# Performance work log

Measured on AMD Instinct MI355X. Metric: run time of the kernel, lower is better.

## Reference

```python
import jax, jax.numpy as jnp
import numpy as np
import math

def _eq_conv1x1(x, w):
    # EqualizedConv2d: 1x1 conv, no bias, weight scaled by sqrt(2 / fan_in) at runtime.
    scale = math.sqrt(2.0 / w.shape[1])
    return jnp.einsum('bchw,oc->bohw', x, w * scale)

def _maxpool2x2(x):
    b, c, h, w = x.shape
    return x.reshape(b, c, h // 2, 2, w // 2, 2).max(axis=(3, 5))

def setup_inputs() -> dict:
    key = jax.random.key(0)
    ks = jax.random.split(key, 6)
    B, Cin, H, W = 8, 256, 64, 64
    Cout = 512
    return {
        'x': jax.random.normal(ks[0], (B, Cin, H, W), dtype=jnp.float32),
        'w_theta': jax.random.normal(ks[1], (Cout // 8, Cin), dtype=jnp.float32),
        'w_phi': jax.random.normal(ks[2], (Cout // 8, Cin), dtype=jnp.float32),
        'w_g': jax.random.normal(ks[3], (Cout // 2, Cin), dtype=jnp.float32),
        'w_o': jax.random.normal(ks[4], (Cout, Cout // 2), dtype=jnp.float32),
        'w_res': jax.random.normal(ks[5], (Cout, Cin), dtype=jnp.float32),
        'gamma': jnp.ones((1,), dtype=jnp.float32),
    }

def reference(x, w_theta, w_phi, w_g, w_o, w_res, gamma):
    B, _, H, W = x.shape
    theta = _eq_conv1x1(x, w_theta).reshape(B, -1, H * W)          # [B, Co/8, HW]
    phi = _maxpool2x2(_eq_conv1x1(x, w_phi)).reshape(B, -1, H * W // 4)  # [B, Co/8, HW/4]
    g = _maxpool2x2(_eq_conv1x1(x, w_g)).reshape(B, -1, H * W // 4)      # [B, Co/2, HW/4]
    # attention: softmax over key dim (no 1/sqrt(d) scaling, as in the original)
    scores = jnp.einsum('bcn,bcm->bnm', theta, phi)                # [B, HW, HW/4]
    beta = jax.nn.softmax(scores, axis=-1)
    att = jnp.einsum('bcm,bnm->bcn', g, beta).reshape(B, -1, H, W)  # [B, Co/2, H, W]
    out = _eq_conv1x1(att, w_o)                                     # [B, Co, H, W]
    res = _eq_conv1x1(x, w_res)
    inv_sqrt2 = jnp.float32(1.0 / math.sqrt(2.0))
    return (gamma[0] * out + res) * inv_sqrt2
```

## Files before the change

kernel.cpp:

```cpp
#include <hip/hip_runtime.h>


typedef _Float16 f16;
typedef f16 f16x2 __attribute__((ext_vector_type(2)));
typedef f16 f16x4 __attribute__((ext_vector_type(4)));
typedef f16 f16x8 __attribute__((ext_vector_type(8)));
typedef float f32x4 __attribute__((ext_vector_type(4)));

#define MFMA16(a, b, c) __builtin_amdgcn_mfma_f32_16x16x32_f16((a), (b), (c), 0, 0, 0)

__device__ __forceinline__ void gload16(const void* src, void* dst_lds) {
  __builtin_amdgcn_global_load_lds(
      (const __attribute__((address_space(1))) void*)src,
      (__attribute__((address_space(3))) void*)dst_lds, 16, 0, 0);
}

__global__ __launch_bounds__(256, 4)
void k_prep_w(const float* __restrict__ wt, const float* __restrict__ wp,
              const float* __restrict__ wg, const float* __restrict__ wo,
              const float* __restrict__ wr, const float* __restrict__ gamma,
              f16* __restrict__ Wproj, f16* __restrict__ Wcat) {
  int i = blockIdx.x * 256 + threadIdx.x;
  const float s = 0.08838834764831845f;
  const float is2 = 0.7071067811865476f;
  if (i < 384 * 256) {
    float v = (i < 64 * 256) ? wt[i]
              : (i < 128 * 256 ? wp[i - 64 * 256] : wg[i - 128 * 256]);
    Wproj[i] = (f16)(v * s);
  } else {
    int j = i - 384 * 256;
    if (j < 512 * 512) {
      int r = j >> 9, c = j & 511;
      float v = (c < 256) ? wo[r * 256 + c] * (gamma[0] * s * is2)
                          : wr[r * 256 + (c - 256)] * (s * is2);
      Wcat[j] = (f16)v;
    }
  }
}

__global__ __launch_bounds__(256, 4)
void k_transpose(const float* __restrict__ x, f16* __restrict__ xT) {
  __shared__ f16 tile[64 * 72];
  int b = blockIdx.z, nt = blockIdx.y, ct = blockIdx.x;
  int t = threadIdx.x;
  {
    int c = t >> 2, nch = (t & 3) * 16;
    const float* src = x + (((size_t)b * 256 + ct * 64 + c) << 12) + nt * 64 + nch;
    float4 v0 = *(const float4*)(src);
    float4 v1 = *(const float4*)(src + 4);
    float4 v2 = *(const float4*)(src + 8);
    float4 v3 = *(const float4*)(src + 12);
    f16x8 a = {(f16)v0.x, (f16)v0.y, (f16)v0.z, (f16)v0.w,
               (f16)v1.x, (f16)v1.y, (f16)v1.z, (f16)v1.w};
    f16x8 bb = {(f16)v2.x, (f16)v2.y, (f16)v2.z, (f16)v2.w,
                (f16)v3.x, (f16)v3.y, (f16)v3.z, (f16)v3.w};
    *(f16x8*)&tile[c * 72 + nch] = a;
    *(f16x8*)&tile[c * 72 + nch + 8] = bb;
  }
  __syncthreads();
  {
    int n = t >> 2, cch = (t & 3) * 16;
    f16 tmp[16];
#pragma unroll
    for (int i = 0; i < 16; i++) tmp[i] = tile[(cch + i) * 72 + n];
    f16x8 a, bb;
#pragma unroll
    for (int i = 0; i < 8; i++) { a[i] = tmp[i]; bb[i] = tmp[8 + i]; }
    f16* dst = xT + (((size_t)b * 4096 + nt * 64 + n) << 8) + ct * 64 + cch;
    *(f16x8*)dst = a;
    *(f16x8*)(dst + 8) = bb;
  }
}

__global__ __launch_bounds__(256, 2)
void k_gemm_projq(const f16* __restrict__ xT, const f16* __restrict__ Wproj,
                  f16* __restrict__ Q, f16* __restrict__ Kp, f16* __restrict__ V) {
  __shared__ f16 lds[192 * 64];
  f16* Alds = lds;
  f16* Blds = lds + 64 * 64;
  int b = blockIdx.z, mt = blockIdx.y, nt = blockIdx.x;
  int tid = threadIdx.x;
  int lane = tid & 63, wave = tid >> 6;
  int wm = wave >> 1, wn = wave & 1;
  int l15 = lane & 15, hi = lane >> 4;
  f32x4 acc[2][4];
#pragma unroll
  for (int mf = 0; mf < 2; mf++)
#pragma unroll
    for (int nf = 0; nf < 4; nf++) acc[mf][nf] = (f32x4){0, 0, 0, 0};
  const f16* Abase = Wproj + ((mt * 64) << 8);
  const f16* Bbase = xT + (((size_t)b * 4096 + nt * 128) << 8);
  for (int k0 = 0; k0 < 256; k0 += 64) {
    __syncthreads();
#pragma unroll
    for (int i = 0; i < 2; i++) {
      int chunk = i * 256 + tid;
      int row = chunk >> 3, cc = chunk & 7, scc = cc ^ (row & 7);
      gload16(Abase + (row << 8) + k0 + scc * 8, (char*)Alds + (i * 256 + wave * 64) * 16);
    }
#pragma unroll
    for (int i = 0; i < 4; i++) {
      int chunk = i * 256 + tid;
      int row = chunk >> 3, cc = chunk & 7, scc = cc ^ (row & 7);
      gload16(Bbase + (row << 8) + k0 + scc * 8, (char*)Blds + (i * 256 + wave * 64) * 16);
    }
    __syncthreads();
#pragma unroll
    for (int ks = 0; ks < 2; ks++) {
      int cb = (hi * 8 + ks * 32) * 2;
      f16x8 af[2], bf[4];
#pragma unroll
      for (int mf = 0; mf < 2; mf++) {
        int row = wm * 32 + mf * 16 + l15;
        af[mf] = *(const f16x8*)((const char*)Alds + row * 128 + (cb ^ ((row & 7) << 4)));
      }
#pragma unroll
      for (int nf = 0; nf < 4; nf++) {
        int row = wn * 64 + nf * 16 + l15;
        bf[nf] = *(const f16x8*)((const char*)Blds + row * 128 + (cb ^ ((row & 7) << 4)));
      }
#pragma unroll
      for (int mf = 0; mf < 2; mf++)
#pragma unroll
        for (int nf = 0; nf < 4; nf++) acc[mf][nf] = MFMA16(af[mf], bf[nf], acc[mf][nf]);
    }
  }
  if (mt == 0) {
#pragma unroll
    for (int mf = 0; mf < 2; mf++)
#pragma unroll
      for (int nf = 0; nf < 4; nf++)
#pragma unroll
        for (int r = 0; r < 4; r++) {
          int jl = wm * 32 + mf * 16 + hi * 4 + r;
          int n = nt * 128 + wn * 64 + nf * 16 + l15;
          Q[(((size_t)b * 4096 + n) << 6) + jl] = (f16)acc[mf][nf][r];
        }
  } else {
    __syncthreads();
    f16* Pool = lds;
#pragma unroll
    for (int mf = 0; mf < 2; mf++)
#pragma unroll
      for (int nf = 0; nf < 4; nf++)
#pragma unroll
        for (int r = 0; r < 4; r++) {
          int jl = wm * 32 + mf * 16 + hi * 4 + r;
          int col = wn * 64 + nf * 16 + l15;
          Pool[jl * 132 + col] = (f16)acc[mf][nf][r];
        }
    __syncthreads();
    if (mt == 1) {
      int m_l = tid >> 3;
      int jj8 = (tid & 7) * 8;
      f16x8 w;
#pragma unroll
      for (int i = 0; i < 8; i++) {
        int jj = jj8 + i;
        f16x2 p0 = *(const f16x2*)&Pool[jj * 132 + 2 * m_l];
        f16x2 p1 = *(const f16x2*)&Pool[jj * 132 + 64 + 2 * m_l];
        float v = fmaxf(fmaxf((float)p0[0], (float)p0[1]),
                        fmaxf((float)p1[0], (float)p1[1]));
        w[i] = (f16)v;
      }
      *(f16x8*)&Kp[((size_t)b * 1024 + nt * 32 + m_l) * 64 + jj8] = w;
    } else {
      int ch_l = tid >> 2;
      int m8 = (tid & 3) * 8;
      f16x8 w;
#pragma unroll
      for (int i = 0; i < 8; i++) {
        int mm = m8 + i;
        f16x2 p0 = *(const f16x2*)&Pool[ch_l * 132 + 2 * mm];
        f16x2 p1 = *(const f16x2*)&Pool[ch_l * 132 + 64 + 2 * mm];
        float v = fmaxf(fmaxf((float)p0[0], (float)p0[1]),
                        fmaxf((float)p1[0], (float)p1[1]));
        w[i] = (f16)v;
      }
      int ch = (mt - 2) * 64 + ch_l;
      *(f16x8*)&V[(((size_t)b * 256 + ch) << 10) + nt * 32 + m8] = w;
    }
  }
}

__global__ __launch_bounds__(512, 4)
void k_flash(const f16* __restrict__ Q, const f16* __restrict__ Kp,
             const f16* __restrict__ V, f16* __restrict__ att) {
  __shared__ f16 Klds[64 * 64];
  __shared__ f16 Vlds[256 * 64];
  __shared__ f16 Plds[4][16 * 72];
  int b = blockIdx.y, qt = blockIdx.x;
  int tid = threadIdx.x;
  int lane = tid & 63, wave = tid >> 6;
  int rg = wave >> 1, cg2 = wave & 1;
  int l15 = lane & 15, hi = lane >> 4;
  const f16* Kb = Kp + ((size_t)b << 16);
  const f16* Vb = V + ((size_t)b << 18);
  f16* Pw = &Plds[rg][0];
  const float L2E = 1.44269504f;
  int krow_s = tid >> 3, kcc = tid & 7;
  int kscc = kcc ^ (krow_s & 7);
  const f16* kp_src = Kb + (krow_s << 6) + kscc * 8;
  f16* kp_dst = &Klds[tid * 8];
  const f16* vp_src[4];
  f16* vp_dst[4];
#pragma unroll
  for (int i = 0; i < 4; i++) {
    int chunk = i * 512 + tid;
    int row = chunk >> 3, cc = chunk & 7, scc = cc ^ (row & 7);
    vp_src[i] = Vb + ((size_t)row << 10) + scc * 8;
    vp_dst[i] = &Vlds[chunk * 8];
  }
  f16x8 qf[2];
#pragma unroll
  for (int ks = 0; ks < 2; ks++)
    qf[ks] = *(const f16x8*)(
        Q + (((size_t)b * 4096 + qt * 64 + rg * 16 + l15) << 6) + ks * 32 + hi * 8);
  f32x4 o[8];
#pragma unroll
  for (int i = 0; i < 8; i++) o[i] = (f32x4){0, 0, 0, 0};
  float mrow = -1e30f, lrow = 0.f;

  int cbase = hi * 16;

  f16x8 kreg, vreg0, vreg1, vreg2, vreg3;
  kreg = *(const f16x8*)(kp_src);
  vreg0 = *(const f16x8*)(vp_src[0]);
  vreg1 = *(const f16x8*)(vp_src[1]);
  vreg2 = *(const f16x8*)(vp_src[2]);
  vreg3 = *(const f16x8*)(vp_src[3]);
  *(f16x8*)kp_dst = kreg;
  *(f16x8*)vp_dst[0] = vreg0;
  *(f16x8*)vp_dst[1] = vreg1;
  *(f16x8*)vp_dst[2] = vreg2;
  *(f16x8*)vp_dst[3] = vreg3;
  __syncthreads();

  for (int kt = 0; kt < 16; ++kt) {
    if (kt < 15) {
      kreg = *(const f16x8*)(kp_src + ((kt + 1) << 12));
      vreg0 = *(const f16x8*)(vp_src[0] + ((kt + 1) << 6));
      vreg1 = *(const f16x8*)(vp_src[1] + ((kt + 1) << 6));
      vreg2 = *(const f16x8*)(vp_src[2] + ((kt + 1) << 6));
      vreg3 = *(const f16x8*)(vp_src[3] + ((kt + 1) << 6));
    }
    f32x4 s[4];
#pragma unroll
    for (int mf = 0; mf < 4; mf++) s[mf] = (f32x4){0, 0, 0, 0};
#pragma unroll
    for (int ks = 0; ks < 2; ks++) {
      f16x8 kf[4];
#pragma unroll
      for (int mf = 0; mf < 4; mf++) {
        int row = mf * 16 + l15;
        kf[mf] = *(const f16x8*)((const char*)&Klds[0] + row * 128 +
                                 ((cbase + ks * 64) ^ ((row & 7) << 4)));
      }
#pragma unroll
      for (int mf = 0; mf < 4; mf++) s[mf] = MFMA16(kf[mf], qf[ks], s[mf]);
    }
    float t0 = fmaxf(fmaxf(s[0][0], s[1][0]), fmaxf(s[2][0], s[3][0]));
    float t1 = fmaxf(fmaxf(s[0][1], s[1][1]), fmaxf(s[2][1], s[3][1]));
    float t2 = fmaxf(fmaxf(s[0][2], s[1][2]), fmaxf(s[2][2], s[3][2]));
    float t3 = fmaxf(fmaxf(s[0][3], s[1][3]), fmaxf(s[2][3], s[3][3]));
    float mx = fmaxf(fmaxf(t0, t1), fmaxf(t2, t3));
    mx = fmaxf(mx, __shfl_xor(mx, 16, 64));
    mx = fmaxf(mx, __shfl_xor(mx, 32, 64));
    if (__any(mx > mrow + 8.f)) {
      float mnew = fmaxf(mrow, mx);
      float corr = __builtin_amdgcn_exp2f((mrow - mnew) * L2E);
      lrow *= corr;
      mrow = mnew;
#pragma unroll
      for (int r = 0; r < 4; r++) {
        float cr = __shfl(corr, (hi << 4) + (hi << 2) + r, 64);
#pragma unroll
        for (int cf = 0; cf < 8; cf++) o[cf][r] *= cr;
      }
    }
    {
      float e[4][4];
#pragma unroll
      for (int mf = 0; mf < 4; mf++)
#pragma unroll
        for (int r = 0; r < 4; r++)
          e[mf][r] = __builtin_amdgcn_exp2f((s[mf][r] - mrow) * L2E);
#pragma unroll
      for (int mf = 0; mf < 4; mf++) {
        f16x4 w = {(f16)e[mf][0], (f16)e[mf][1], (f16)e[mf][2], (f16)e[mf][3]};
        *(f16x4*)((char*)Pw + l15 * 144 + mf * 32 + hi * 8) = w;
      }
      float u0 = (e[0][0] + e[1][0]) + (e[2][0] + e[3][0]);
      float u1 = (e[0][1] + e[1][1]) + (e[2][1] + e[3][1]);
      float u2 = (e[0][2] + e[1][2]) + (e[2][2] + e[3][2]);
      float u3 = (e[0][3] + e[1][3]) + (e[2][3] + e[3][3]);
      float sum = (u0 + u1) + (u2 + u3);
      sum += __shfl_xor(sum, 16, 64);
      sum += __shfl_xor(sum, 32, 64);
      lrow += sum;
    }
#pragma unroll
    for (int ks = 0; ks < 2; ks++) {
      f16x8 af = *(const f16x8*)((char*)Pw + l15 * 144 + ks * 64 + hi * 16);
      __builtin_amdgcn_s_setprio(1);
#pragma unroll
      for (int cg = 0; cg < 2; cg++) {
        f16x8 vf[4];
#pragma unroll
        for (int u = 0; u < 4; u++) {
          int row = (cg2 * 8 + cg * 4 + u) * 16 + l15;
          vf[u] = *(const f16x8*)((const char*)&Vlds[0] + row * 128 +
                                  ((cbase + ks * 64) ^ ((row & 7) << 4)));
        }
#pragma unroll
        for (int u = 0; u < 4; u++) o[cg * 4 + u] = MFMA16(af, vf[u], o[cg * 4 + u]);
      }
      __builtin_amdgcn_s_setprio(0);
    }
    if (kt < 15) {
      __syncthreads();
      *(f16x8*)kp_dst = kreg;
      *(f16x8*)vp_dst[0] = vreg0;
      *(f16x8*)vp_dst[1] = vreg1;
      *(f16x8*)vp_dst[2] = vreg2;
      *(f16x8*)vp_dst[3] = vreg3;
      __syncthreads();
    }
  }
  int nbase = qt * 64 + rg * 16 + hi * 4;
  float inv = 1.f / lrow;
#pragma unroll
  for (int r = 0; r < 4; r++) {
    float iv = __shfl(inv, (hi << 4) + (hi << 2) + r, 64);
#pragma unroll
    for (int cf = 0; cf < 8; cf++) {
      int n = nbase + r;
      int c = cg2 * 128 + cf * 16 + l15;
      att[(((size_t)b * 4096 + n) << 8) + c] = (f16)(o[cf][r] * iv);
    }
  }
}

__global__ __launch_bounds__(256, 2)
void k_gemm_out(const f16* __restrict__ Wcat, const f16* __restrict__ att,
                const f16* __restrict__ xT, float* __restrict__ out) {
  __shared__ f16 Alds[128 * 64];
  __shared__ f16 Blds[128 * 64];
  int b = blockIdx.z, mt = blockIdx.y, nt = blockIdx.x;
  int lane = threadIdx.x & 63, wave = threadIdx.x >> 6;
  int wm = wave >> 1, wn = wave & 1;
  f32x4 acc[4][4];
#pragma unroll
  for (int mf = 0; mf < 4; mf++)
#pragma unroll
    for (int nf = 0; nf < 4; nf++) acc[mf][nf] = (f32x4){0, 0, 0, 0};
  const f16* Abase = Wcat + (size_t)(mt * 128) * 512;
  for (int k0 = 0; k0 < 512; k0 += 64) {
    __syncthreads();
#pragma unroll
    for (int i = 0; i < 4; i++) {
      int chunk = i * 256 + threadIdx.x;
      int row = chunk >> 3, cc = chunk & 7, scc = cc ^ (row & 7);
      gload16(Abase + row * 512 + k0 + scc * 8, (char*)Alds + (i * 256 + wave * 64) * 16);
    }
    const f16* Bcol = (k0 < 256) ? (att + (((size_t)b * 4096 + nt * 128) << 8))
                                 : (xT + (((size_t)b * 4096 + nt * 128) << 8));
    int kk = (k0 < 256) ? k0 : (k0 - 256);
#pragma unroll
    for (int i = 0; i < 4; i++) {
      int chunk = i * 256 + threadIdx.x;
      int row = chunk >> 3, cc = chunk & 7, scc = cc ^ (row & 7);
      gload16(Bcol + (row << 8) + kk + scc * 8, (char*)Blds + (i * 256 + wave * 64) * 16);
    }
    __syncthreads();
#pragma unroll
    for (int ks = 0; ks < 2; ks++) {
      int cb = ((lane >> 4) * 8 + ks * 32) * 2;
      f16x8 af[4], bf[4];
#pragma unroll
      for (int mf = 0; mf < 4; mf++) {
        int row = wm * 64 + mf * 16 + (lane & 15);
        af[mf] = *(const f16x8*)((const char*)Alds + row * 128 + (cb ^ ((row & 7) << 4)));
      }
#pragma unroll
      for (int nf = 0; nf < 4; nf++) {
        int row = wn * 64 + nf * 16 + (lane & 15);
        bf[nf] = *(const f16x8*)((const char*)Blds + row * 128 + (cb ^ ((row & 7) << 4)));
      }
#pragma unroll
      for (int mf = 0; mf < 4; mf++)
#pragma unroll
        for (int nf = 0; nf < 4; nf++) acc[mf][nf] = MFMA16(af[mf], bf[nf], acc[mf][nf]);
    }
  }
#pragma unroll
  for (int mf = 0; mf < 4; mf++)
#pragma unroll
    for (int nf = 0; nf < 4; nf++)
#pragma unroll
      for (int r = 0; r < 4; r++) {
        int oo = mt * 128 + wm * 64 + mf * 16 + (lane >> 4) * 4 + r;
        int n = nt * 128 + wn * 64 + nf * 16 + (lane & 15);
        out[(((size_t)b * 512 + oo) << 12) + n] = acc[mf][nf][r];
      }
}

extern "C" void kernel_launch(void* const* d_in, const int* in_sizes, int n_in,
                              void* d_out, int out_size, void* d_ws, size_t ws_size,
                              hipStream_t stream) {
  const float* x = (const float*)d_in[0];
  const float* wt = (const float*)d_in[1];
  const float* wp = (const float*)d_in[2];
  const float* wg = (const float*)d_in[3];
  const float* wo = (const float*)d_in[4];
  const float* wr = (const float*)d_in[5];
  const float* gm = (const float*)d_in[6];
  float* out = (float*)d_out;
  char* ws = (char*)d_ws;
  const size_t MB = 1024 * 1024;
  f16* xT = (f16*)(ws);
  f16* Qb = (f16*)(ws + 16 * MB);
  f16* Kp = (f16*)(ws + 20 * MB);
  f16* Vb = (f16*)(ws + 21 * MB);
  f16* Wproj = (f16*)(ws + 25 * MB);
  f16* Wcat = (f16*)(ws + 25 * MB + 512 * 1024);
  f16* att = (f16*)(ws + 26 * MB);

  hipLaunchKernelGGL(k_prep_w, dim3(1408), dim3(256), 0, stream, wt, wp, wg, wo, wr, gm,
                     Wproj, Wcat);
  hipLaunchKernelGGL(k_transpose, dim3(4, 64, 8), dim3(256), 0, stream, x, xT);
  hipLaunchKernelGGL(k_gemm_projq, dim3(32, 6, 8), dim3(256), 0, stream, xT, Wproj, Qb,
                     Kp, Vb);
  hipLaunchKernelGGL(k_flash, dim3(64, 8), dim3(512), 0, stream, Qb, Kp, Vb, att);
  hipLaunchKernelGGL(k_gemm_out, dim3(32, 4, 8), dim3(256), 0, stream, Wcat, att, xT, out);
}
```

Before: 107.6 us.

## Fuse output projection and residual GEMM into flash attention epilogue

The separate output GEMM kernel is removed. Each flash block now writes its normalized attention tile into shared memory, loads the matching xT tile, and multiplies both by the concatenated output/residual weight to write the final result directly. The weight matrix is pre-packed into an MFMA-fragment layout so each wave can read A fragments straight from global memory without staging them in shared memory. This drops the att round trip through global memory and one kernel launch. In exchange the flash kernel grows its shared-memory footprint and register pressure, and every block re-reads the full 512x512 weight from global memory or cache.

```diff
diff --git a/kernel.cpp b/kernel.cpp
--- a/kernel.cpp
+++ b/kernel.cpp
@@ -19,7 +19,7 @@
 void k_prep_w(const float* __restrict__ wt, const float* __restrict__ wp,
               const float* __restrict__ wg, const float* __restrict__ wo,
               const float* __restrict__ wr, const float* __restrict__ gamma,
-              f16* __restrict__ Wproj, f16* __restrict__ Wcat) {
+              f16* __restrict__ Wproj, f16* __restrict__ WcatP) {
   int i = blockIdx.x * 256 + threadIdx.x;
   const float s = 0.08838834764831845f;
   const float is2 = 0.7071067811865476f;
@@ -33,7 +33,8 @@
       int r = j >> 9, c = j & 511;
       float v = (c < 256) ? wo[r * 256 + c] * (gamma[0] * s * is2)
                           : wr[r * 256 + (c - 256)] * (s * is2);
-      Wcat[j] = (f16)v;
+      int og = r >> 4, lr = r & 15, kc = c >> 5, h2 = (c >> 3) & 3, e = c & 7;
+      WcatP[(((og * 16 + kc) * 64 + h2 * 16 + lr) << 3) + e] = (f16)v;
     }
   }
 }
@@ -185,10 +186,12 @@
 
 __global__ __launch_bounds__(512, 4)
 void k_flash(const f16* __restrict__ Q, const f16* __restrict__ Kp,
-             const f16* __restrict__ V, f16* __restrict__ att) {
-  __shared__ f16 Klds[64 * 64];
-  __shared__ f16 Vlds[256 * 64];
-  __shared__ f16 Plds[4][16 * 72];
+             const f16* __restrict__ V, const f16* __restrict__ xT,
+             const f16* __restrict__ WcatP, float* __restrict__ out) {
+  __shared__ char smem[65536];
+  f16* Klds = (f16*)smem;
+  f16* Vlds = (f16*)(smem + 8192);
+  f16* PldsB = (f16*)(smem + 40960);
   int b = blockIdx.y, qt = blockIdx.x;
   int tid = threadIdx.x;
   int lane = tid & 63, wave = tid >> 6;
@@ -196,7 +199,7 @@
   int l15 = lane & 15, hi = lane >> 4;
   const f16* Kb = Kp + ((size_t)b << 16);
   const f16* Vb = V + ((size_t)b << 18);
-  f16* Pw = &Plds[rg][0];
+  f16* Pw = PldsB + rg * 16 * 72;
   const float L2E = 1.44269504f;
   int krow_s = tid >> 3, kcc = tid & 7;
   int kscc = kcc ^ (krow_s & 7);
@@ -253,7 +256,7 @@
 #pragma unroll
       for (int mf = 0; mf < 4; mf++) {
         int row = mf * 16 + l15;
-        kf[mf] = *(const f16x8*)((const char*)&Klds[0] + row * 128 +
+        kf[mf] = *(const f16x8*)((const char*)Klds + row * 128 +
                                  ((cbase + ks * 64) ^ ((row & 7) << 4)));
       }
 #pragma unroll
@@ -309,7 +312,7 @@
 #pragma unroll
         for (int u = 0; u < 4; u++) {
           int row = (cg2 * 8 + cg * 4 + u) * 16 + l15;
-          vf[u] = *(const f16x8*)((const char*)&Vlds[0] + row * 128 +
+          vf[u] = *(const f16x8*)((const char*)Vlds + row * 128 +
                                   ((cbase + ks * 64) ^ ((row & 7) << 4)));
         }
 #pragma unroll
@@ -327,82 +330,69 @@
       __syncthreads();
     }
   }
-  int nbase = qt * 64 + rg * 16 + hi * 4;
-  float inv = 1.f / lrow;
-#pragma unroll
-  for (int r = 0; r < 4; r++) {
-    float iv = __shfl(inv, (hi << 4) + (hi << 2) + r, 64);
-#pragma unroll
-    for (int cf = 0; cf < 8; cf++) {
-      int n = nbase + r;
-      int c = cg2 * 128 + cf * 16 + l15;
-      att[(((size_t)b * 4096 + n) << 8) + c] = (f16)(o[cf][r] * iv);
-    }
-  }
-}
-
-__global__ __launch_bounds__(256, 2)
-void k_gemm_out(const f16* __restrict__ Wcat, const f16* __restrict__ att,
-                const f16* __restrict__ xT, float* __restrict__ out) {
-  __shared__ f16 Alds[128 * 64];
-  __shared__ f16 Blds[128 * 64];
-  int b = blockIdx.z, mt = blockIdx.y, nt = blockIdx.x;
-  int lane = threadIdx.x & 63, wave = threadIdx.x >> 6;
-  int wm = wave >> 1, wn = wave & 1;
-  f32x4 acc[4][4];
-#pragma unroll
-  for (int mf = 0; mf < 4; mf++)
-#pragma unroll
-    for (int nf = 0; nf < 4; nf++) acc[mf][nf] = (f32x4){0, 0, 0, 0};
-  const f16* Abase = Wcat + (size_t)(mt * 128) * 512;
-  for (int k0 = 0; k0 < 512; k0 += 64) {
-    __syncthreads();
-#pragma unroll
-    for (int i = 0; i < 4; i++) {
-      int chunk = i * 256 + threadIdx.x;
-      int row = chunk >> 3, cc = chunk & 7, scc = cc ^ (row & 7);
-      gload16(Abase + row * 512 + k0 + scc * 8, (char*)Alds + (i * 256 + wave * 64) * 16);
-    }
-    const f16* Bcol = (k0 < 256) ? (att + (((size_t)b * 4096 + nt * 128) << 8))
-                                 : (xT + (((size_t)b * 4096 + nt * 128) << 8));
-    int kk = (k0 < 256) ? k0 : (k0 - 256);
-#pragma unroll
-    for (int i = 0; i < 4; i++) {
-      int chunk = i * 256 + threadIdx.x;
-      int row = chunk >> 3, cc = chunk & 7, scc = cc ^ (row & 7);
-      gload16(Bcol + (row << 8) + kk + scc * 8, (char*)Blds + (i * 256 + wave * 64) * 16);
-    }
-    __syncthreads();
-#pragma unroll
-    for (int ks = 0; ks < 2; ks++) {
-      int cb = ((lane >> 4) * 8 + ks * 32) * 2;
+
+  __syncthreads();
+  f16* attT = (f16*)smem;
+  f16* xTT = (f16*)(smem + 32768);
+#pragma unroll
+  for (int i = 0; i < 4; i++) {
+    int chunk = i * 512 + tid;
+    int row = chunk >> 5, cc = chunk & 31, scc = cc ^ (row & 7);
+    gload16(xT + (((size_t)b * 4096 + qt * 64 + row) << 8) + scc * 8,
+            (char*)xTT + chunk * 16);
+  }
+  {
+    float inv = 1.f / lrow;
+    int nb = rg * 16 + hi * 4;
+#pragma unroll
+    for (int r = 0; r < 4; r++) {
+      float iv = __shfl(inv, (hi << 4) + (hi << 2) + r, 64);
+      int n = nb + r;
+#pragma unroll
+      for (int cf = 0; cf < 8; cf++) {
+        int c = cg2 * 128 + cf * 16 + l15;
+        *(f16*)((char*)attT + n * 512 + ((c * 2) ^ ((n & 7) << 4))) =
+            (f16)(o[cf][r] * iv);
+      }
+    }
+  }
+  __syncthreads();
+  {
+    f32x4 acc2[4][4];
+#pragma unroll
+    for (int mf = 0; mf < 4; mf++)
+#pragma unroll
+      for (int nf = 0; nf < 4; nf++) acc2[mf][nf] = (f32x4){0, 0, 0, 0};
+    for (int kc = 0; kc < 16; ++kc) {
+      const char* tile = (kc < 8) ? (const char*)attT : (const char*)xTT;
+      int ub = (kc & 7) * 64 + hi * 16;
       f16x8 af[4], bf[4];
 #pragma unroll
-      for (int mf = 0; mf < 4; mf++) {
-        int row = wm * 64 + mf * 16 + (lane & 15);
-        af[mf] = *(const f16x8*)((const char*)Alds + row * 128 + (cb ^ ((row & 7) << 4)));
-      }
+      for (int mf = 0; mf < 4; mf++)
+        af[mf] = *(const f16x8*)(WcatP +
+                                 ((size_t)(((wave * 4 + mf) * 16 + kc) * 64 + lane) << 3));
 #pragma unroll
       for (int nf = 0; nf < 4; nf++) {
-        int row = wn * 64 + nf * 16 + (lane & 15);
-        bf[nf] = *(const f16x8*)((const char*)Blds + row * 128 + (cb ^ ((row & 7) << 4)));
+        int row = nf * 16 + l15;
+        bf[nf] = *(const f16x8*)(tile + row * 512 + (ub ^ ((row & 7) << 4)));
       }
 #pragma unroll
       for (int mf = 0; mf < 4; mf++)
 #pragma unroll
-        for (int nf = 0; nf < 4; nf++) acc[mf][nf] = MFMA16(af[mf], bf[nf], acc[mf][nf]);
-    }
-  }
-#pragma unroll
-  for (int mf = 0; mf < 4; mf++)
-#pragma unroll
-    for (int nf = 0; nf < 4; nf++)
-#pragma unroll
-      for (int r = 0; r < 4; r++) {
-        int oo = mt * 128 + wm * 64 + mf * 16 + (lane >> 4) * 4 + r;
-        int n = nt * 128 + wn * 64 + nf * 16 + (lane & 15);
-        out[(((size_t)b * 512 + oo) << 12) + n] = acc[mf][nf][r];
-      }
+        for (int nf = 0; nf < 4; nf++)
+          acc2[mf][nf] = MFMA16(af[mf], bf[nf], acc2[mf][nf]);
+    }
+#pragma unroll
+    for (int mf = 0; mf < 4; mf++)
+#pragma unroll
+      for (int nf = 0; nf < 4; nf++)
+#pragma unroll
+        for (int r = 0; r < 4; r++) {
+          int oo = wave * 64 + mf * 16 + hi * 4 + r;
+          int n = qt * 64 + nf * 16 + l15;
+          out[(((size_t)b * 512 + oo) << 12) + n] = acc2[mf][nf][r];
+        }
+  }
 }
 
 extern "C" void kernel_launch(void* const* d_in, const int* in_sizes, int n_in,
@@ -423,14 +413,13 @@
   f16* Kp = (f16*)(ws + 20 * MB);
   f16* Vb = (f16*)(ws + 21 * MB);
   f16* Wproj = (f16*)(ws + 25 * MB);
-  f16* Wcat = (f16*)(ws + 25 * MB + 512 * 1024);
-  f16* att = (f16*)(ws + 26 * MB);
+  f16* WcatP = (f16*)(ws + 25 * MB + 512 * 1024);
 
   hipLaunchKernelGGL(k_prep_w, dim3(1408), dim3(256), 0, stream, wt, wp, wg, wo, wr, gm,
-                     Wproj, Wcat);
+                     Wproj, WcatP);
   hipLaunchKernelGGL(k_transpose, dim3(4, 64, 8), dim3(256), 0, stream, x, xT);
   hipLaunchKernelGGL(k_gemm_projq, dim3(32, 6, 8), dim3(256), 0, stream, xT, Wproj, Qb,
                      Kp, Vb);
-  hipLaunchKernelGGL(k_flash, dim3(64, 8), dim3(512), 0, stream, Qb, Kp, Vb, att);
-  hipLaunchKernelGGL(k_gemm_out, dim3(32, 4, 8), dim3(256), 0, stream, Wcat, att, xT, out);
-}
+  hipLaunchKernelGGL(k_flash, dim3(64, 8), dim3(512), 0, stream, Qb, Kp, Vb, xT, WcatP,
+                     out);
+}
```

Result: faster. 97.57 us (-9.4%).
